# Kernel optimization log

Measured on AMD Instinct MI355X. Metric: run time of the kernel, lower is better.

## Reference

```python
import jax, jax.numpy as jnp
import numpy as np

N_NODES = 50000
D = 128
BN_EPS = 1e-5
GIN_EPS = 0.0  # GINConv default eps


def setup_inputs() -> dict:
    key = jax.random.key(0)
    ks = jax.random.split(key, 8)
    feature = jax.random.normal(ks[0], (N_NODES, D), dtype=jnp.float32)
    edge_index = jax.random.randint(ks[1], (2, 600000), 0, N_NODES, dtype=jnp.int32)
    s = 1.0 / np.sqrt(D)
    W1 = jax.random.uniform(ks[2], (D, D), jnp.float32, -s, s)
    b1 = jax.random.uniform(ks[3], (D,), jnp.float32, -s, s)
    W2 = jax.random.uniform(ks[4], (D, D), jnp.float32, -s, s)
    b2 = jax.random.uniform(ks[5], (D,), jnp.float32, -s, s)
    gamma = jnp.ones((D,), jnp.float32)
    beta = jnp.zeros((D,), jnp.float32)
    return {"feature": feature, "edge_index": edge_index,
            "W1": W1, "b1": b1, "W2": W2, "b2": b2,
            "gamma": gamma, "beta": beta}


def reference(feature, edge_index, W1, b1, W2, b2, gamma, beta):
    src, dst = edge_index[0], edge_index[1]
    # GIN aggregation: sum of neighbor (source) features at each target node
    agg = jax.ops.segment_sum(feature[src], dst, num_segments=N_NODES)
    h = (1.0 + GIN_EPS) * feature + agg
    # 2-layer MLP
    h = jax.nn.relu(h @ W1 + b1) @ W2 + b2
    # outer ReLU
    y = jax.nn.relu(h)
    # BatchNorm1d (training mode: batch statistics, biased variance)
    mean = jnp.mean(y, axis=0)
    var = jnp.mean(jnp.square(y - mean), axis=0)
    out = (y - mean) * jax.lax.rsqrt(var + BN_EPS) * gamma + beta
    return out
```

## Files before the change

### kernel.cpp

```cpp
#include <hip/hip_runtime.h>

#define N_NODES 50000
#define D 128
#define N_EDGES 600000
#define BN_EPS 1e-5f
#define NREP 64
#define BUCKET 64

#define MLP_BLOCKS 512
#define N_GROUPS   3125
#define MLP_WAVES  (MLP_BLOCKS * 4)

#define FEATC_BLOCKS 3125
#define WPREP_BLOCKS 128
#define ZERO_BLOCKS  260

typedef __attribute__((ext_vector_type(8))) short short8;
typedef __attribute__((ext_vector_type(4))) float floatx4;

__device__ __forceinline__ unsigned f2bf(float f) {
    unsigned x = __float_as_uint(f);
    return (x + 0x7fffu + ((x >> 16) & 1u)) >> 16;
}
__device__ __forceinline__ float bflo(unsigned v) { return __uint_as_float(v << 16); }
__device__ __forceinline__ float bfhi(unsigned v) { return __uint_as_float(v & 0xffff0000u); }

__global__ void prep_kernel(const float* __restrict__ f, unsigned* __restrict__ fb,
                            const float* __restrict__ W1, const float* __restrict__ W2,
                            unsigned short* __restrict__ Wt1, unsigned short* __restrict__ Wt2,
                            int* __restrict__ cnt, float* __restrict__ stats) {
    int b = blockIdx.x;
    int tid = threadIdx.x;
    if (b < FEATC_BLOCKS) {
        int gid = b * 256 + tid;
        float4 a = ((const float4*)f)[gid * 2];
        float4 c = ((const float4*)f)[gid * 2 + 1];
        uint4 o;
        o.x = f2bf(a.x) | (f2bf(a.y) << 16);
        o.y = f2bf(a.z) | (f2bf(a.w) << 16);
        o.z = f2bf(c.x) | (f2bf(c.y) << 16);
        o.w = f2bf(c.z) | (f2bf(c.w) << 16);
        ((uint4*)fb)[gid] = o;
    } else if (b < FEATC_BLOCKS + WPREP_BLOCKS) {
        int gid = (b - FEATC_BLOCKS) * 256 + tid;
        int m = gid >> 14;
        int idx = gid & (D * D - 1);
        int k = idx >> 7;
        int n = idx & 127;
        const float* W = m ? W2 : W1;
        unsigned short* Wt = m ? Wt2 : Wt1;
        Wt[n * D + k] = (unsigned short)f2bf(W[k * D + n]);
    } else {
        int gid = (b - FEATC_BLOCKS - WPREP_BLOCKS) * 256 + tid;
        if (gid < N_NODES) cnt[gid] = 0;
        int sid = gid - N_NODES;
        if (sid >= 0 && sid < NREP * 256) stats[sid] = 0.f;
    }
}

__global__ void scatter_kernel(const int* __restrict__ ei,
                               int* __restrict__ cnt,
                               unsigned short* __restrict__ ssrc) {
    int e = blockIdx.x * blockDim.x + threadIdx.x;
    if (e >= N_EDGES) return;
    int src = ei[e];
    int dst = ei[N_EDGES + e];
    int pos = atomicAdd(&cnt[dst], 1);
    ssrc[dst * BUCKET + pos] = (unsigned short)src;
}

__global__ __launch_bounds__(256) void gather_kernel(const uint4* __restrict__ fb4,
                                                     const int* __restrict__ cnt,
                                                     const unsigned short* __restrict__ ssrc,
                                                     uint4* __restrict__ hb4) {
    int wave = (blockIdx.x * 256 + threadIdx.x) >> 6;
    int lane = threadIdx.x & 63;
    int quad = lane >> 4;
    int l16 = lane & 15;
    int node = wave * 4 + quad;
    int beg = node * BUCKET;
    int end = beg + cnt[node];

    float a0, a1, a2, a3, a4, a5, a6, a7;
    uint4 own = fb4[node * 16 + l16];
    a0 = bflo(own.x); a1 = bfhi(own.x);
    a2 = bflo(own.y); a3 = bfhi(own.y);
    a4 = bflo(own.z); a5 = bfhi(own.z);
    a6 = bflo(own.w); a7 = bfhi(own.w);

    int j = beg;
    for (; j + 3 < end; j += 4) {
        uint4 v0 = fb4[(int)ssrc[j] * 16 + l16];
        uint4 v1 = fb4[(int)ssrc[j + 1] * 16 + l16];
        uint4 v2 = fb4[(int)ssrc[j + 2] * 16 + l16];
        uint4 v3 = fb4[(int)ssrc[j + 3] * 16 + l16];
        a0 += (bflo(v0.x) + bflo(v1.x)) + (bflo(v2.x) + bflo(v3.x));
        a1 += (bfhi(v0.x) + bfhi(v1.x)) + (bfhi(v2.x) + bfhi(v3.x));
        a2 += (bflo(v0.y) + bflo(v1.y)) + (bflo(v2.y) + bflo(v3.y));
        a3 += (bfhi(v0.y) + bfhi(v1.y)) + (bfhi(v2.y) + bfhi(v3.y));
        a4 += (bflo(v0.z) + bflo(v1.z)) + (bflo(v2.z) + bflo(v3.z));
        a5 += (bfhi(v0.z) + bfhi(v1.z)) + (bfhi(v2.z) + bfhi(v3.z));
        a6 += (bflo(v0.w) + bflo(v1.w)) + (bflo(v2.w) + bflo(v3.w));
        a7 += (bfhi(v0.w) + bfhi(v1.w)) + (bfhi(v2.w) + bfhi(v3.w));
    }
    for (; j < end; ++j) {
        uint4 v = fb4[(int)ssrc[j] * 16 + l16];
        a0 += bflo(v.x); a1 += bfhi(v.x);
        a2 += bflo(v.y); a3 += bfhi(v.y);
        a4 += bflo(v.z); a5 += bfhi(v.z);
        a6 += bflo(v.w); a7 += bfhi(v.w);
    }

    uint4 o;
    o.x = f2bf(a0) | (f2bf(a1) << 16);
    o.y = f2bf(a2) | (f2bf(a3) << 16);
    o.z = f2bf(a4) | (f2bf(a5) << 16);
    o.w = f2bf(a6) | (f2bf(a7) << 16);
    hb4[node * 16 + l16] = o;
}

__global__ __launch_bounds__(256) void mlp_kernel(
    const unsigned short* __restrict__ A,
    const unsigned short* __restrict__ Bt1, const unsigned short* __restrict__ Bt2,
    const float* __restrict__ bias1, const float* __restrict__ bias2,
    unsigned short* __restrict__ yb, float* __restrict__ stats)
{
    __shared__ unsigned short B1lds[128 * 128];
    __shared__ unsigned short B2lds[128 * 128];
    __shared__ unsigned short Xch[4 * 16 * 128];

    const int tid = threadIdx.x;

    #pragma unroll
    for (int i = 0; i < 8; ++i) {
        int c = tid + i * 256;
        int row = c >> 4;
        int g = c & 15;
        int dst = row * 128 + (g ^ (row & 15)) * 8;
        int src = row * 128 + g * 8;
        *(uint4*)&B1lds[dst] = *(const uint4*)&Bt1[src];
        *(uint4*)&B2lds[dst] = *(const uint4*)&Bt2[src];
    }
    __syncthreads();

    const int lane = tid & 63;
    const int wid = tid >> 6;
    const int l15 = lane & 15;
    const int quad = lane >> 4;
    unsigned short* X = &Xch[wid * 2048];

    float bs1[8], bs2[8];
    #pragma unroll
    for (int n = 0; n < 8; ++n) {
        bs1[n] = bias1[n * 16 + l15];
        bs2[n] = bias2[n * 16 + l15];
    }

    float s[8], q[8];
    #pragma unroll
    for (int n = 0; n < 8; ++n) { s[n] = 0.f; q[n] = 0.f; }

    const int gw = blockIdx.x * 4 + wid;
    for (int grp = gw; grp < N_GROUPS; grp += MLP_WAVES) {
        const int rowBase = grp * 16;

        short8 af[4];
        #pragma unroll
        for (int kc = 0; kc < 4; ++kc)
            af[kc] = *(const short8*)&A[(rowBase + l15) * 128 + kc * 32 + quad * 8];

        floatx4 acc[8];
        #pragma unroll
        for (int n = 0; n < 8; ++n) acc[n] = (floatx4){0.f, 0.f, 0.f, 0.f};
        #pragma unroll
        for (int kc = 0; kc < 4; ++kc) {
            int ga = (kc * 4 + quad) ^ l15;
            #pragma unroll
            for (int n = 0; n < 8; ++n) {
                short8 bf = *(const short8*)&B1lds[(n * 16 + l15) * 128 + ga * 8];
                acc[n] = __builtin_amdgcn_mfma_f32_16x16x32_bf16(af[kc], bf, acc[n], 0, 0, 0);
            }
        }

        #pragma unroll
        for (int n = 0; n < 8; ++n) {
            int col = n * 16 + l15;
            int gg = col >> 3;
            int o7 = col & 7;
            #pragma unroll
            for (int r = 0; r < 4; ++r) {
                int rl = quad * 4 + r;
                float v = fmaxf(acc[n][r] + bs1[n], 0.f);
                X[rl * 128 + ((gg ^ rl) * 8) + o7] = (unsigned short)f2bf(v);
            }
        }
        #pragma unroll
        for (int kc = 0; kc < 4; ++kc)
            af[kc] = *(const short8*)&X[l15 * 128 + (((kc * 4 + quad) ^ l15) * 8)];

        #pragma unroll
        for (int n = 0; n < 8; ++n) acc[n] = (floatx4){0.f, 0.f, 0.f, 0.f};
        #pragma unroll
        for (int kc = 0; kc < 4; ++kc) {
            int ga = (kc * 4 + quad) ^ l15;
            #pragma unroll
            for (int n = 0; n < 8; ++n) {
                short8 bf = *(const short8*)&B2lds[(n * 16 + l15) * 128 + ga * 8];
                acc[n] = __builtin_amdgcn_mfma_f32_16x16x32_bf16(af[kc], bf, acc[n], 0, 0, 0);
            }
        }

        #pragma unroll
        for (int n = 0; n < 8; ++n) {
            int col = n * 16 + l15;
            #pragma unroll
            for (int r = 0; r < 4; ++r) {
                int row = rowBase + quad * 4 + r;
                float v = fmaxf(acc[n][r] + bs2[n], 0.f);
                yb[row * 128 + col] = (unsigned short)f2bf(v);
                s[n] += v;
                q[n] += v * v;
            }
        }
    }

    #pragma unroll
    for (int n = 0; n < 8; ++n) {
        s[n] += __shfl_xor(s[n], 16);
        s[n] += __shfl_xor(s[n], 32);
        q[n] += __shfl_xor(q[n], 16);
        q[n] += __shfl_xor(q[n], 32);
    }
    __syncthreads();
    float* red = (float*)B1lds;
    if (lane < 16) {
        #pragma unroll
        for (int n = 0; n < 8; ++n) {
            red[wid * 128 + n * 16 + lane] = s[n];
            red[512 + wid * 128 + n * 16 + lane] = q[n];
        }
    }
    __syncthreads();
    float* myStats = stats + (blockIdx.x & (NREP - 1)) * 256;
    if (tid < 128) {
        float ss = 0.f, qq = 0.f;
        #pragma unroll
        for (int w = 0; w < 4; ++w) {
            ss += red[w * 128 + tid];
            qq += red[512 + w * 128 + tid];
        }
        atomicAdd(&myStats[tid], ss);
        atomicAdd(&myStats[128 + tid], qq);
    }
}

__global__ __launch_bounds__(256) void bn_kernel(const uint4* __restrict__ yb4,
                                                 float* __restrict__ out,
                                                 const float* __restrict__ stats,
                                                 const float* __restrict__ gamma,
                                                 const float* __restrict__ beta)
{
    __shared__ float red[256];
    __shared__ float sc[128], sh[128];
    int tid = threadIdx.x;

    float acc = 0.f;
    #pragma unroll 8
    for (int r = 0; r < NREP; ++r) acc += stats[r * 256 + tid];
    red[tid] = acc;
    __syncthreads();
    if (tid < 128) {
        const float inv_n = 1.0f / (float)N_NODES;
        float m = red[tid] * inv_n;
        float var = red[128 + tid] * inv_n - m * m;
        float scale = gamma[tid] * rsqrtf(var + BN_EPS);
        sc[tid] = scale;
        sh[tid] = beta[tid] - m * scale;
    }
    __syncthreads();

    const int n8 = N_NODES * D / 8;
    int base = (blockIdx.x * 256 + tid) * 4;
    #pragma unroll
    for (int i = 0; i < 4; ++i) {
        int idx = base + i;
        if (idx >= n8) break;
        int c0 = (idx << 3) & 127;
        uint4 v = yb4[idx];
        float4 o0, o1;
        o0.x = bflo(v.x) * sc[c0 + 0] + sh[c0 + 0];
        o0.y = bfhi(v.x) * sc[c0 + 1] + sh[c0 + 1];
        o0.z = bflo(v.y) * sc[c0 + 2] + sh[c0 + 2];
        o0.w = bfhi(v.y) * sc[c0 + 3] + sh[c0 + 3];
        o1.x = bflo(v.z) * sc[c0 + 4] + sh[c0 + 4];
        o1.y = bfhi(v.z) * sc[c0 + 5] + sh[c0 + 5];
        o1.z = bflo(v.w) * sc[c0 + 6] + sh[c0 + 6];
        o1.w = bfhi(v.w) * sc[c0 + 7] + sh[c0 + 7];
        ((float4*)out)[idx * 2] = o0;
        ((float4*)out)[idx * 2 + 1] = o1;
    }
}

extern "C" void kernel_launch(void* const* d_in, const int* in_sizes, int n_in,
                              void* d_out, int out_size, void* d_ws, size_t ws_size,
                              hipStream_t stream) {
    const float* feature = (const float*)d_in[0];
    const int*   ei      = (const int*)d_in[1];
    const float* W1      = (const float*)d_in[2];
    const float* b1      = (const float*)d_in[3];
    const float* W2      = (const float*)d_in[4];
    const float* b2      = (const float*)d_in[5];
    const float* gamma   = (const float*)d_in[6];
    const float* beta    = (const float*)d_in[7];
    float* out = (float*)d_out;

    unsigned*       featb = (unsigned*)d_ws;
    unsigned*       hb    = featb + N_NODES * 64;
    unsigned*       yb32  = hb + N_NODES * 64;
    unsigned short* Wt1   = (unsigned short*)(yb32 + N_NODES * 64);
    unsigned short* Wt2   = Wt1 + D * D;
    float*          stats = (float*)(Wt2 + D * D);
    int*            cnt   = (int*)(stats + NREP * 256);
    unsigned short* ssrc  = (unsigned short*)(cnt + N_NODES);
    unsigned short* yb    = (unsigned short*)yb32;

    prep_kernel<<<FEATC_BLOCKS + WPREP_BLOCKS + ZERO_BLOCKS, 256, 0, stream>>>(
        feature, featb, W1, W2, Wt1, Wt2, cnt, stats);
    scatter_kernel<<<(N_EDGES + 255) / 256, 256, 0, stream>>>(ei, cnt, ssrc);
    gather_kernel<<<N_NODES / 4 * 64 / 256, 256, 0, stream>>>(
        (const uint4*)featb, cnt, ssrc, (uint4*)hb);
    mlp_kernel<<<MLP_BLOCKS, 256, 0, stream>>>(
        (const unsigned short*)hb, Wt1, Wt2, b1, b2, yb, stats);
    bn_kernel<<<(N_NODES * D / 8 / 4 + 255) / 256, 256, 0, stream>>>(
        (const uint4*)yb, out, stats, gamma, beta);
}
```

Baseline: 182.3 us.

## Fuse neighbor gather into MLP kernel with atomic ticket work distribution

Removes the standalone gather kernel and does the neighbor aggregation inside the MLP kernel. Each wave sums features for its 16-row group and writes the bf16 result straight into a swizzled LDS tile that feeds the MFMA A operand. This avoids writing the intermediate aggregated features to global memory and reading them back, and removes one kernel launch. Groups are now handed out through an atomic ticket counter that prep_kernel zeroes, and neighbor indices are loaded eight at a time as vectors. The risk is lower memory parallelism during the gather, since only a few LDS-heavy MLP blocks fit per CU and each quad walks its four nodes one after another.

```diff
diff --git a/kernel.cpp b/kernel.cpp
--- a/kernel.cpp
+++ b/kernel.cpp
@@ -9,11 +9,10 @@
 
 #define MLP_BLOCKS 512
 #define N_GROUPS   3125
-#define MLP_WAVES  (MLP_BLOCKS * 4)
 
 #define FEATC_BLOCKS 3125
 #define WPREP_BLOCKS 128
-#define ZERO_BLOCKS  260
+#define ZERO_BLOCKS  261
 
 typedef __attribute__((ext_vector_type(8))) short short8;
 typedef __attribute__((ext_vector_type(4))) float floatx4;
@@ -54,7 +53,7 @@
         int gid = (b - FEATC_BLOCKS - WPREP_BLOCKS) * 256 + tid;
         if (gid < N_NODES) cnt[gid] = 0;
         int sid = gid - N_NODES;
-        if (sid >= 0 && sid < NREP * 256) stats[sid] = 0.f;
+        if (sid >= 0 && sid < NREP * 256 + 256) stats[sid] = 0.f;
     }
 }
 
@@ -69,61 +68,14 @@
     ssrc[dst * BUCKET + pos] = (unsigned short)src;
 }
 
-__global__ __launch_bounds__(256) void gather_kernel(const uint4* __restrict__ fb4,
-                                                     const int* __restrict__ cnt,
-                                                     const unsigned short* __restrict__ ssrc,
-                                                     uint4* __restrict__ hb4) {
-    int wave = (blockIdx.x * 256 + threadIdx.x) >> 6;
-    int lane = threadIdx.x & 63;
-    int quad = lane >> 4;
-    int l16 = lane & 15;
-    int node = wave * 4 + quad;
-    int beg = node * BUCKET;
-    int end = beg + cnt[node];
-
-    float a0, a1, a2, a3, a4, a5, a6, a7;
-    uint4 own = fb4[node * 16 + l16];
-    a0 = bflo(own.x); a1 = bfhi(own.x);
-    a2 = bflo(own.y); a3 = bfhi(own.y);
-    a4 = bflo(own.z); a5 = bfhi(own.z);
-    a6 = bflo(own.w); a7 = bfhi(own.w);
-
-    int j = beg;
-    for (; j + 3 < end; j += 4) {
-        uint4 v0 = fb4[(int)ssrc[j] * 16 + l16];
-        uint4 v1 = fb4[(int)ssrc[j + 1] * 16 + l16];
-        uint4 v2 = fb4[(int)ssrc[j + 2] * 16 + l16];
-        uint4 v3 = fb4[(int)ssrc[j + 3] * 16 + l16];
-        a0 += (bflo(v0.x) + bflo(v1.x)) + (bflo(v2.x) + bflo(v3.x));
-        a1 += (bfhi(v0.x) + bfhi(v1.x)) + (bfhi(v2.x) + bfhi(v3.x));
-        a2 += (bflo(v0.y) + bflo(v1.y)) + (bflo(v2.y) + bflo(v3.y));
-        a3 += (bfhi(v0.y) + bfhi(v1.y)) + (bfhi(v2.y) + bfhi(v3.y));
-        a4 += (bflo(v0.z) + bflo(v1.z)) + (bflo(v2.z) + bflo(v3.z));
-        a5 += (bfhi(v0.z) + bfhi(v1.z)) + (bfhi(v2.z) + bfhi(v3.z));
-        a6 += (bflo(v0.w) + bflo(v1.w)) + (bflo(v2.w) + bflo(v3.w));
-        a7 += (bfhi(v0.w) + bfhi(v1.w)) + (bfhi(v2.w) + bfhi(v3.w));
-    }
-    for (; j < end; ++j) {
-        uint4 v = fb4[(int)ssrc[j] * 16 + l16];
-        a0 += bflo(v.x); a1 += bfhi(v.x);
-        a2 += bflo(v.y); a3 += bfhi(v.y);
-        a4 += bflo(v.z); a5 += bfhi(v.z);
-        a6 += bflo(v.w); a7 += bfhi(v.w);
-    }
-
-    uint4 o;
-    o.x = f2bf(a0) | (f2bf(a1) << 16);
-    o.y = f2bf(a2) | (f2bf(a3) << 16);
-    o.z = f2bf(a4) | (f2bf(a5) << 16);
-    o.w = f2bf(a6) | (f2bf(a7) << 16);
-    hb4[node * 16 + l16] = o;
-}
-
 __global__ __launch_bounds__(256) void mlp_kernel(
-    const unsigned short* __restrict__ A,
+    const uint4* __restrict__ fb4,
+    const int* __restrict__ cnt,
+    const unsigned short* __restrict__ ssrc,
     const unsigned short* __restrict__ Bt1, const unsigned short* __restrict__ Bt2,
     const float* __restrict__ bias1, const float* __restrict__ bias2,
-    unsigned short* __restrict__ yb, float* __restrict__ stats)
+    unsigned short* __restrict__ yb, float* __restrict__ stats,
+    int* __restrict__ ticket)
 {
     __shared__ unsigned short B1lds[128 * 128];
     __shared__ unsigned short B2lds[128 * 128];
@@ -160,14 +112,76 @@
     #pragma unroll
     for (int n = 0; n < 8; ++n) { s[n] = 0.f; q[n] = 0.f; }
 
-    const int gw = blockIdx.x * 4 + wid;
-    for (int grp = gw; grp < N_GROUPS; grp += MLP_WAVES) {
+    for (;;) {
+        int grp = 0;
+        if (lane == 0) grp = atomicAdd(ticket, 1);
+        grp = __shfl(grp, 0);
+        if (grp >= N_GROUPS) break;
         const int rowBase = grp * 16;
 
+        #pragma unroll
+        for (int t = 0; t < 4; ++t) {
+            const int rl = quad * 4 + t;
+            const int node = rowBase + rl;
+            const int beg = node * BUCKET;
+            const int end = beg + cnt[node];
+
+            uint4 own = fb4[node * 16 + l15];
+            float a0 = bflo(own.x), a1 = bfhi(own.x);
+            float a2 = bflo(own.y), a3 = bfhi(own.y);
+            float a4 = bflo(own.z), a5 = bfhi(own.z);
+            float a6 = bflo(own.w), a7 = bfhi(own.w);
+
+            int j = beg;
+            #define ACC8(v) do { \
+                a0 += bflo((v).x); a1 += bfhi((v).x); \
+                a2 += bflo((v).y); a3 += bfhi((v).y); \
+                a4 += bflo((v).z); a5 += bfhi((v).z); \
+                a6 += bflo((v).w); a7 += bfhi((v).w); } while (0)
+            for (; j + 7 < end; j += 8) {
+                uint4 sv = *(const uint4*)&ssrc[j];
+                int i0 = sv.x & 0xffff, i1 = sv.x >> 16;
+                int i2 = sv.y & 0xffff, i3 = sv.y >> 16;
+                int i4 = sv.z & 0xffff, i5 = sv.z >> 16;
+                int i6 = sv.w & 0xffff, i7 = sv.w >> 16;
+                uint4 v0 = fb4[i0 * 16 + l15];
+                uint4 v1 = fb4[i1 * 16 + l15];
+                uint4 v2 = fb4[i2 * 16 + l15];
+                uint4 v3 = fb4[i3 * 16 + l15];
+                uint4 v4 = fb4[i4 * 16 + l15];
+                uint4 v5 = fb4[i5 * 16 + l15];
+                uint4 v6 = fb4[i6 * 16 + l15];
+                uint4 v7 = fb4[i7 * 16 + l15];
+                ACC8(v0); ACC8(v1); ACC8(v2); ACC8(v3);
+                ACC8(v4); ACC8(v5); ACC8(v6); ACC8(v7);
+            }
+            if (j + 3 < end) {
+                ushort4 sv = *(const ushort4*)&ssrc[j];
+                uint4 v0 = fb4[(int)sv.x * 16 + l15];
+                uint4 v1 = fb4[(int)sv.y * 16 + l15];
+                uint4 v2 = fb4[(int)sv.z * 16 + l15];
+                uint4 v3 = fb4[(int)sv.w * 16 + l15];
+                ACC8(v0); ACC8(v1); ACC8(v2); ACC8(v3);
+                j += 4;
+            }
+            for (; j < end; ++j) {
+                uint4 v = fb4[(int)ssrc[j] * 16 + l15];
+                ACC8(v);
+            }
+            #undef ACC8
+
+            uint4 o;
+            o.x = f2bf(a0) | (f2bf(a1) << 16);
+            o.y = f2bf(a2) | (f2bf(a3) << 16);
+            o.z = f2bf(a4) | (f2bf(a5) << 16);
+            o.w = f2bf(a6) | (f2bf(a7) << 16);
+            *(uint4*)&X[rl * 128 + ((l15 ^ rl) * 8)] = o;
+        }
+
         short8 af[4];
         #pragma unroll
         for (int kc = 0; kc < 4; ++kc)
-            af[kc] = *(const short8*)&A[(rowBase + l15) * 128 + kc * 32 + quad * 8];
+            af[kc] = *(const short8*)&X[l15 * 128 + (((kc * 4 + quad) ^ l15) * 8)];
 
         floatx4 acc[8];
         #pragma unroll
@@ -315,22 +329,20 @@
     float* out = (float*)d_out;
 
     unsigned*       featb = (unsigned*)d_ws;
-    unsigned*       hb    = featb + N_NODES * 64;
-    unsigned*       yb32  = hb + N_NODES * 64;
+    unsigned*       yb32  = featb + N_NODES * 64;
     unsigned short* Wt1   = (unsigned short*)(yb32 + N_NODES * 64);
     unsigned short* Wt2   = Wt1 + D * D;
     float*          stats = (float*)(Wt2 + D * D);
-    int*            cnt   = (int*)(stats + NREP * 256);
+    int*            ticket= (int*)(stats + NREP * 256);
+    int*            cnt   = ticket + 256;
     unsigned short* ssrc  = (unsigned short*)(cnt + N_NODES);
     unsigned short* yb    = (unsigned short*)yb32;
 
     prep_kernel<<<FEATC_BLOCKS + WPREP_BLOCKS + ZERO_BLOCKS, 256, 0, stream>>>(
         feature, featb, W1, W2, Wt1, Wt2, cnt, stats);
     scatter_kernel<<<(N_EDGES + 255) / 256, 256, 0, stream>>>(ei, cnt, ssrc);
-    gather_kernel<<<N_NODES / 4 * 64 / 256, 256, 0, stream>>>(
-        (const uint4*)featb, cnt, ssrc, (uint4*)hb);
     mlp_kernel<<<MLP_BLOCKS, 256, 0, stream>>>(
-        (const unsigned short*)hb, Wt1, Wt2, b1, b2, yb, stats);
+        (const uint4*)featb, cnt, ssrc, Wt1, Wt2, b1, b2, yb, stats, ticket);
     bn_kernel<<<(N_NODES * D / 8 / 4 + 255) / 256, 256, 0, stream>>>(
         (const uint4*)yb, out, stats, gamma, beta);
 }
```

Measured after the change: 226.1 us. 24.1% more time.

## Fuse BatchNorm into MLP kernel via grid barrier and widen gather index loads

Applied to the files above, without the earlier changes.

Removes the separate BN kernel. Each MLP wave now processes at most two fixed row groups and keeps their post-ReLU outputs packed in registers. A spin-wait grid barrier on an atomic counter follows the stats reduction, after which each block applies the normalization and writes fp32 output directly. This drops the bf16 intermediate y round-trip and one launch. The gather loop also loads eight source indices per 128-bit read and unrolls eight neighbors. The barrier assumes all 512 blocks are co-resident and has a spin-limit escape that could yield wrong stats if it trips.

```diff
diff --git a/kernel.cpp b/kernel.cpp
--- a/kernel.cpp
+++ b/kernel.cpp
@@ -8,8 +8,8 @@
 #define BUCKET 64
 
 #define MLP_BLOCKS 512
+#define MLP_WAVES  (MLP_BLOCKS * 4)
 #define N_GROUPS   3125
-#define MLP_WAVES  (MLP_BLOCKS * 4)
 
 #define FEATC_BLOCKS 3125
 #define WPREP_BLOCKS 128
@@ -54,7 +54,7 @@
         int gid = (b - FEATC_BLOCKS - WPREP_BLOCKS) * 256 + tid;
         if (gid < N_NODES) cnt[gid] = 0;
         int sid = gid - N_NODES;
-        if (sid >= 0 && sid < NREP * 256) stats[sid] = 0.f;
+        if (sid >= 0 && sid < NREP * 256 + 64) stats[sid] = 0.f;
     }
 }
 
@@ -81,35 +81,49 @@
     int beg = node * BUCKET;
     int end = beg + cnt[node];
 
-    float a0, a1, a2, a3, a4, a5, a6, a7;
     uint4 own = fb4[node * 16 + l16];
-    a0 = bflo(own.x); a1 = bfhi(own.x);
-    a2 = bflo(own.y); a3 = bfhi(own.y);
-    a4 = bflo(own.z); a5 = bfhi(own.z);
-    a6 = bflo(own.w); a7 = bfhi(own.w);
+    float a0 = bflo(own.x), a1 = bfhi(own.x);
+    float a2 = bflo(own.y), a3 = bfhi(own.y);
+    float a4 = bflo(own.z), a5 = bfhi(own.z);
+    float a6 = bflo(own.w), a7 = bfhi(own.w);
 
     int j = beg;
-    for (; j + 3 < end; j += 4) {
-        uint4 v0 = fb4[(int)ssrc[j] * 16 + l16];
-        uint4 v1 = fb4[(int)ssrc[j + 1] * 16 + l16];
-        uint4 v2 = fb4[(int)ssrc[j + 2] * 16 + l16];
-        uint4 v3 = fb4[(int)ssrc[j + 3] * 16 + l16];
-        a0 += (bflo(v0.x) + bflo(v1.x)) + (bflo(v2.x) + bflo(v3.x));
-        a1 += (bfhi(v0.x) + bfhi(v1.x)) + (bfhi(v2.x) + bfhi(v3.x));
-        a2 += (bflo(v0.y) + bflo(v1.y)) + (bflo(v2.y) + bflo(v3.y));
-        a3 += (bfhi(v0.y) + bfhi(v1.y)) + (bfhi(v2.y) + bfhi(v3.y));
-        a4 += (bflo(v0.z) + bflo(v1.z)) + (bflo(v2.z) + bflo(v3.z));
-        a5 += (bfhi(v0.z) + bfhi(v1.z)) + (bfhi(v2.z) + bfhi(v3.z));
-        a6 += (bflo(v0.w) + bflo(v1.w)) + (bflo(v2.w) + bflo(v3.w));
-        a7 += (bfhi(v0.w) + bfhi(v1.w)) + (bfhi(v2.w) + bfhi(v3.w));
+    #define ACC8(v) do { \
+        a0 += bflo((v).x); a1 += bfhi((v).x); \
+        a2 += bflo((v).y); a3 += bfhi((v).y); \
+        a4 += bflo((v).z); a5 += bfhi((v).z); \
+        a6 += bflo((v).w); a7 += bfhi((v).w); } while (0)
+    for (; j + 7 < end; j += 8) {
+        uint4 sv = *(const uint4*)&ssrc[j];
+        int i0 = sv.x & 0xffff, i1 = sv.x >> 16;
+        int i2 = sv.y & 0xffff, i3 = sv.y >> 16;
+        int i4 = sv.z & 0xffff, i5 = sv.z >> 16;
+        int i6 = sv.w & 0xffff, i7 = sv.w >> 16;
+        uint4 v0 = fb4[i0 * 16 + l16];
+        uint4 v1 = fb4[i1 * 16 + l16];
+        uint4 v2 = fb4[i2 * 16 + l16];
+        uint4 v3 = fb4[i3 * 16 + l16];
+        uint4 v4 = fb4[i4 * 16 + l16];
+        uint4 v5 = fb4[i5 * 16 + l16];
+        uint4 v6 = fb4[i6 * 16 + l16];
+        uint4 v7 = fb4[i7 * 16 + l16];
+        ACC8(v0); ACC8(v1); ACC8(v2); ACC8(v3);
+        ACC8(v4); ACC8(v5); ACC8(v6); ACC8(v7);
+    }
+    if (j + 3 < end) {
+        ushort4 sv = *(const ushort4*)&ssrc[j];
+        uint4 v0 = fb4[(int)sv.x * 16 + l16];
+        uint4 v1 = fb4[(int)sv.y * 16 + l16];
+        uint4 v2 = fb4[(int)sv.z * 16 + l16];
+        uint4 v3 = fb4[(int)sv.w * 16 + l16];
+        ACC8(v0); ACC8(v1); ACC8(v2); ACC8(v3);
+        j += 4;
     }
     for (; j < end; ++j) {
         uint4 v = fb4[(int)ssrc[j] * 16 + l16];
-        a0 += bflo(v.x); a1 += bfhi(v.x);
-        a2 += bflo(v.y); a3 += bfhi(v.y);
-        a4 += bflo(v.z); a5 += bfhi(v.z);
-        a6 += bflo(v.w); a7 += bfhi(v.w);
-    }
+        ACC8(v);
+    }
+    #undef ACC8
 
     uint4 o;
     o.x = f2bf(a0) | (f2bf(a1) << 16);
@@ -123,7 +137,9 @@
     const unsigned short* __restrict__ A,
     const unsigned short* __restrict__ Bt1, const unsigned short* __restrict__ Bt2,
     const float* __restrict__ bias1, const float* __restrict__ bias2,
-    unsigned short* __restrict__ yb, float* __restrict__ stats)
+    float* __restrict__ stats, int* __restrict__ done,
+    const float* __restrict__ gamma, const float* __restrict__ beta,
+    float* __restrict__ out)
 {
     __shared__ unsigned short B1lds[128 * 128];
     __shared__ unsigned short B2lds[128 * 128];
@@ -160,67 +176,76 @@
     #pragma unroll
     for (int n = 0; n < 8; ++n) { s[n] = 0.f; q[n] = 0.f; }
 
+    unsigned ypk[2][8][2];
+
     const int gw = blockIdx.x * 4 + wid;
-    for (int grp = gw; grp < N_GROUPS; grp += MLP_WAVES) {
-        const int rowBase = grp * 16;
-
-        short8 af[4];
-        #pragma unroll
-        for (int kc = 0; kc < 4; ++kc)
-            af[kc] = *(const short8*)&A[(rowBase + l15) * 128 + kc * 32 + quad * 8];
-
-        floatx4 acc[8];
-        #pragma unroll
-        for (int n = 0; n < 8; ++n) acc[n] = (floatx4){0.f, 0.f, 0.f, 0.f};
-        #pragma unroll
-        for (int kc = 0; kc < 4; ++kc) {
-            int ga = (kc * 4 + quad) ^ l15;
+
+    #pragma unroll
+    for (int g = 0; g < 2; ++g) {
+        const int grp = gw + g * MLP_WAVES;
+        if (grp < N_GROUPS) {
+            const int rowBase = grp * 16;
+
+            short8 af[4];
+            #pragma unroll
+            for (int kc = 0; kc < 4; ++kc)
+                af[kc] = *(const short8*)&A[(rowBase + l15) * 128 + kc * 32 + quad * 8];
+
+            floatx4 acc[8];
+            #pragma unroll
+            for (int n = 0; n < 8; ++n) acc[n] = (floatx4){0.f, 0.f, 0.f, 0.f};
+            #pragma unroll
+            for (int kc = 0; kc < 4; ++kc) {
+                int ga = (kc * 4 + quad) ^ l15;
+                #pragma unroll
+                for (int n = 0; n < 8; ++n) {
+                    short8 bf = *(const short8*)&B1lds[(n * 16 + l15) * 128 + ga * 8];
+                    acc[n] = __builtin_amdgcn_mfma_f32_16x16x32_bf16(af[kc], bf, acc[n], 0, 0, 0);
+                }
+            }
+
             #pragma unroll
             for (int n = 0; n < 8; ++n) {
-                short8 bf = *(const short8*)&B1lds[(n * 16 + l15) * 128 + ga * 8];
-                acc[n] = __builtin_amdgcn_mfma_f32_16x16x32_bf16(af[kc], bf, acc[n], 0, 0, 0);
+                int col = n * 16 + l15;
+                int gg = col >> 3;
+                int o7 = col & 7;
+                #pragma unroll
+                for (int r = 0; r < 4; ++r) {
+                    int rl = quad * 4 + r;
+                    float v = fmaxf(acc[n][r] + bs1[n], 0.f);
+                    X[rl * 128 + ((gg ^ rl) * 8) + o7] = (unsigned short)f2bf(v);
+                }
             }
-        }
-
-        #pragma unroll
-        for (int n = 0; n < 8; ++n) {
-            int col = n * 16 + l15;
-            int gg = col >> 3;
-            int o7 = col & 7;
-            #pragma unroll
-            for (int r = 0; r < 4; ++r) {
-                int rl = quad * 4 + r;
-                float v = fmaxf(acc[n][r] + bs1[n], 0.f);
-                X[rl * 128 + ((gg ^ rl) * 8) + o7] = (unsigned short)f2bf(v);
+            #pragma unroll
+            for (int kc = 0; kc < 4; ++kc)
+                af[kc] = *(const short8*)&X[l15 * 128 + (((kc * 4 + quad) ^ l15) * 8)];
+
+            #pragma unroll
+            for (int n = 0; n < 8; ++n) acc[n] = (floatx4){0.f, 0.f, 0.f, 0.f};
+            #pragma unroll
+            for (int kc = 0; kc < 4; ++kc) {
+                int ga = (kc * 4 + quad) ^ l15;
+                #pragma unroll
+                for (int n = 0; n < 8; ++n) {
+                    short8 bf = *(const short8*)&B2lds[(n * 16 + l15) * 128 + ga * 8];
+                    acc[n] = __builtin_amdgcn_mfma_f32_16x16x32_bf16(af[kc], bf, acc[n], 0, 0, 0);
+                }
             }
-        }
-        #pragma unroll
-        for (int kc = 0; kc < 4; ++kc)
-            af[kc] = *(const short8*)&X[l15 * 128 + (((kc * 4 + quad) ^ l15) * 8)];
-
-        #pragma unroll
-        for (int n = 0; n < 8; ++n) acc[n] = (floatx4){0.f, 0.f, 0.f, 0.f};
-        #pragma unroll
-        for (int kc = 0; kc < 4; ++kc) {
-            int ga = (kc * 4 + quad) ^ l15;
+
             #pragma unroll
             for (int n = 0; n < 8; ++n) {
-                short8 bf = *(const short8*)&B2lds[(n * 16 + l15) * 128 + ga * 8];
-                acc[n] = __builtin_amdgcn_mfma_f32_16x16x32_bf16(af[kc], bf, acc[n], 0, 0, 0);
+                float v0 = fmaxf(acc[n][0] + bs2[n], 0.f);
+                float v1 = fmaxf(acc[n][1] + bs2[n], 0.f);
+                float v2 = fmaxf(acc[n][2] + bs2[n], 0.f);
+                float v3 = fmaxf(acc[n][3] + bs2[n], 0.f);
+                s[n] += (v0 + v1) + (v2 + v3);
+                q[n] += (v0 * v0 + v1 * v1) + (v2 * v2 + v3 * v3);
+                ypk[g][n][0] = f2bf(v0) | (f2bf(v1) << 16);
+                ypk[g][n][1] = f2bf(v2) | (f2bf(v3) << 16);
             }
-        }
-
-        #pragma unroll
-        for (int n = 0; n < 8; ++n) {
-            int col = n * 16 + l15;
-            #pragma unroll
-            for (int r = 0; r < 4; ++r) {
-                int row = rowBase + quad * 4 + r;
-                float v = fmaxf(acc[n][r] + bs2[n], 0.f);
-                yb[row * 128 + col] = (unsigned short)f2bf(v);
-                s[n] += v;
-                q[n] += v * v;
-            }
+        } else {
+            #pragma unroll
+            for (int n = 0; n < 8; ++n) { ypk[g][n][0] = 0; ypk[g][n][1] = 0; }
         }
     }
 
@@ -252,23 +277,28 @@
         atomicAdd(&myStats[tid], ss);
         atomicAdd(&myStats[128 + tid], qq);
     }
-}
-
-__global__ __launch_bounds__(256) void bn_kernel(const uint4* __restrict__ yb4,
-                                                 float* __restrict__ out,
-                                                 const float* __restrict__ stats,
-                                                 const float* __restrict__ gamma,
-                                                 const float* __restrict__ beta)
-{
-    __shared__ float red[256];
-    __shared__ float sc[128], sh[128];
-    int tid = threadIdx.x;
-
-    float acc = 0.f;
+
+    __syncthreads();
+    if (tid == 0) {
+        __threadfence();
+        atomicAdd(done, 1);
+        int spins = 0;
+        while (__hip_atomic_load(done, __ATOMIC_RELAXED, __HIP_MEMORY_SCOPE_AGENT)
+               < MLP_BLOCKS) {
+            if (++spins > (1 << 20)) break;
+            __builtin_amdgcn_s_sleep(2);
+        }
+        __threadfence();
+    }
+    __syncthreads();
+
+    float accs = 0.f;
     #pragma unroll 8
-    for (int r = 0; r < NREP; ++r) acc += stats[r * 256 + tid];
-    red[tid] = acc;
-    __syncthreads();
+    for (int r = 0; r < NREP; ++r) accs += stats[r * 256 + tid];
+    red[tid] = accs;
+    __syncthreads();
+    float* sc = (float*)B2lds;
+    float* sh = sc + 128;
     if (tid < 128) {
         const float inv_n = 1.0f / (float)N_NODES;
         float m = red[tid] * inv_n;
@@ -279,25 +309,22 @@
     }
     __syncthreads();
 
-    const int n8 = N_NODES * D / 8;
-    int base = (blockIdx.x * 256 + tid) * 4;
-    #pragma unroll
-    for (int i = 0; i < 4; ++i) {
-        int idx = base + i;
-        if (idx >= n8) break;
-        int c0 = (idx << 3) & 127;
-        uint4 v = yb4[idx];
-        float4 o0, o1;
-        o0.x = bflo(v.x) * sc[c0 + 0] + sh[c0 + 0];
-        o0.y = bfhi(v.x) * sc[c0 + 1] + sh[c0 + 1];
-        o0.z = bflo(v.y) * sc[c0 + 2] + sh[c0 + 2];
-        o0.w = bfhi(v.y) * sc[c0 + 3] + sh[c0 + 3];
-        o1.x = bflo(v.z) * sc[c0 + 4] + sh[c0 + 4];
-        o1.y = bfhi(v.z) * sc[c0 + 5] + sh[c0 + 5];
-        o1.z = bflo(v.w) * sc[c0 + 6] + sh[c0 + 6];
-        o1.w = bfhi(v.w) * sc[c0 + 7] + sh[c0 + 7];
-        ((float4*)out)[idx * 2] = o0;
-        ((float4*)out)[idx * 2 + 1] = o1;
+    #pragma unroll
+    for (int g = 0; g < 2; ++g) {
+        const int grp = gw + g * MLP_WAVES;
+        if (grp >= N_GROUPS) continue;
+        const int rowBase = grp * 16 + quad * 4;
+        #pragma unroll
+        for (int n = 0; n < 8; ++n) {
+            int col = n * 16 + l15;
+            float scc = sc[col], shh = sh[col];
+            float v0 = bflo(ypk[g][n][0]), v1 = bfhi(ypk[g][n][0]);
+            float v2 = bflo(ypk[g][n][1]), v3 = bfhi(ypk[g][n][1]);
+            out[(rowBase + 0) * 128 + col] = v0 * scc + shh;
+            out[(rowBase + 1) * 128 + col] = v1 * scc + shh;
+            out[(rowBase + 2) * 128 + col] = v2 * scc + shh;
+            out[(rowBase + 3) * 128 + col] = v3 * scc + shh;
+        }
     }
 }
 
@@ -316,13 +343,12 @@
 
     unsigned*       featb = (unsigned*)d_ws;
     unsigned*       hb    = featb + N_NODES * 64;
-    unsigned*       yb32  = hb + N_NODES * 64;
-    unsigned short* Wt1   = (unsigned short*)(yb32 + N_NODES * 64);
+    unsigned short* Wt1   = (unsigned short*)(hb + N_NODES * 64);
     unsigned short* Wt2   = Wt1 + D * D;
     float*          stats = (float*)(Wt2 + D * D);
-    int*            cnt   = (int*)(stats + NREP * 256);
+    int*            done  = (int*)(stats + NREP * 256);
+    int*            cnt   = done + 64;
     unsigned short* ssrc  = (unsigned short*)(cnt + N_NODES);
-    unsigned short* yb    = (unsigned short*)yb32;
 
     prep_kernel<<<FEATC_BLOCKS + WPREP_BLOCKS + ZERO_BLOCKS, 256, 0, stream>>>(
         feature, featb, W1, W2, Wt1, Wt2, cnt, stats);
@@ -330,7 +356,5 @@
     gather_kernel<<<N_NODES / 4 * 64 / 256, 256, 0, stream>>>(
         (const uint4*)featb, cnt, ssrc, (uint4*)hb);
     mlp_kernel<<<MLP_BLOCKS, 256, 0, stream>>>(
-        (const unsigned short*)hb, Wt1, Wt2, b1, b2, yb, stats);
-    bn_kernel<<<(N_NODES * D / 8 / 4 + 255) / 256, 256, 0, stream>>>(
-        (const uint4*)yb, out, stats, gamma, beta);
-}
+        (const unsigned short*)hb, Wt1, Wt2, b1, b2, stats, done, gamma, beta, out);
+}
```

Result: slower. 200.2 us (+9.8%).
